# Kernel optimization log

Measured on AMD Instinct MI355X. Metric: run time of the kernel, lower is better.

Reference implementation:

```python
import jax, jax.numpy as jnp
import numpy as np

V, E, H, B, T1, T2 = 32000, 300, 300, 64, 48, 48


def _lstm_last(x, Wih, Whh, bih, bhh):
    # x: [T, B, in]; returns final hidden state h_T: [B, H] (PyTorch gate order i,f,g,o)
    h0 = jnp.zeros((x.shape[1], Whh.shape[1]), x.dtype)
    def step(carry, xt):
        h, c = carry
        g = xt @ Wih.T + h @ Whh.T + bih + bhh
        i, f, gc, o = jnp.split(g, 4, axis=-1)
        c = jax.nn.sigmoid(f) * c + jax.nn.sigmoid(i) * jnp.tanh(gc)
        h = jax.nn.sigmoid(o) * jnp.tanh(c)
        return (h, c), None
    (h, _), _ = jax.lax.scan(step, (h0, h0), x)
    return h


def _bilstm_last(x, pf, pr):
    hf = _lstm_last(x, *pf)
    hr = _lstm_last(x[::-1], *pr)
    # faithful quirk: original reverses projr[0] along dim 0 == BATCH dim
    return jnp.concatenate([hf, hr[::-1]], axis=1)  # [B, 2H]


def _forward(x1, x2, x1_mask, x2_mask,
             emb, eW, eU, ebi, ebh, rW, rU, rbi, rbh,
             dW, dU, dbi, dbh, sW, sU, sbi, sbh,
             f1w, f1b, f2w, f2b, fow, fob):
    emb1 = emb[x1]  # [T1,B,E]
    emb2 = emb[x2]
    # encoder outputs final hidden [B,2H], broadcast over time by mask multiply (faithful quirk)
    ctx1 = _bilstm_last(emb1, (eW, eU, ebi, ebh), (rW, rU, rbi, rbh))[None] * x1_mask[:, :, None]  # [T1,B,2H]
    ctx2 = _bilstm_last(emb2, (eW, eU, ebi, ebh), (rW, rU, rbi, rbh))[None] * x2_mask[:, :, None]  # [T2,B,2H]
    c1 = ctx1.transpose(1, 0, 2)  # [B,T1,2H]
    c2 = ctx2.transpose(1, 0, 2)  # [B,T2,2H]
    # scores[b,i,j] = max_d c1[b,i,d]*c2[b,j,d]  (vectorized form of the O(T1*T2) python loop)
    scores = jnp.max(c1[:, :, None, :] * c2[:, None, :, :], axis=-1)  # [B,T1,T2]
    m1 = x1_mask.T  # [B,T1]
    m2 = x2_mask.T  # [B,T2]
    # masked softmax over hypothesis axis (axis=2)
    ea = jnp.exp(scores - jnp.max(scores, axis=2, keepdims=True)) * m2[:, None, :]
    alpha = ea / jnp.sum(ea, axis=2, keepdims=True)  # [B,T1,T2]
    # faithful quirk: MAX (not sum) pooling of attention-weighted hypothesis
    a_tilde = jnp.max(alpha[:, :, :, None] * c2[:, None, :, :], axis=2)  # [B,T1,2H]
    # masked softmax over premise axis (axis=1)
    eb = jnp.exp(scores - jnp.max(scores, axis=1, keepdims=True)) * m1[:, :, None]
    beta = eb / jnp.sum(eb, axis=1, keepdims=True)  # [B,T1,T2]
    b_tilde = jnp.einsum('bij,bid->bjd', beta, c1)  # [B,T2,2H]
    ctx1_ = a_tilde.transpose(1, 0, 2)  # [T1,B,2H]
    ctx2_ = b_tilde.transpose(1, 0, 2)  # [T2,B,2H]
    inp1 = jnp.concatenate([ctx1, ctx1_, ctx1 * ctx1_, ctx1 - ctx1_], axis=2)  # [T1,B,8H]
    inp2 = jnp.concatenate([ctx2, ctx2_, ctx2 * ctx2_, ctx2 - ctx2_], axis=2)
    h1 = jax.nn.relu(inp1 @ f1w.T + f1b)
    h2 = jax.nn.relu(inp2 @ f1w.T + f1b)
    ctx3 = _bilstm_last(h1, (dW, dU, dbi, dbh), (sW, sU, sbi, sbh))  # [B,2H]
    ctx4 = _bilstm_last(h2, (dW, dU, dbi, dbh), (sW, sU, sbi, sbh))  # [B,2H]
    w3 = ctx3[None] * x1_mask[:, :, None]  # [T1,B,2H]
    w4 = ctx4[None] * x2_mask[:, :, None]  # [T2,B,2H]
    logit = jnp.concatenate([
        w3.sum(0) / x1_mask.sum(0)[:, None], w3.max(0),
        w4.sum(0) / x2_mask.sum(0)[:, None], w4.max(0)], axis=1)  # [B,8H]
    logit = jnp.tanh(logit @ f2w.T + f2b)
    return logit @ fow.T + fob  # [B,3]


def setup_inputs() -> dict:
    key = jax.random.key(0)
    ks = jax.random.split(key, 32)
    s = 0.05
    n = lambda k, shape: jax.random.normal(k, shape, jnp.float32) * s
    d = {
        'x1': jax.random.randint(ks[0], (T1, B), 0, V, dtype=jnp.int32),
        'x1_mask': jnp.ones((T1, B), jnp.float32),
        'x2': jax.random.randint(ks[1], (T2, B), 0, V, dtype=jnp.int32),
        'x2_mask': jnp.ones((T2, B), jnp.float32),
        'l': T1,
        'embed_table': n(ks[2], (V, E)),
        'enc_Wih': n(ks[3], (4 * H, E)), 'enc_Whh': n(ks[4], (4 * H, H)),
        'enc_bih': n(ks[5], (4 * H,)), 'enc_bhh': n(ks[6], (4 * H,)),
        'encr_Wih': n(ks[7], (4 * H, E)), 'encr_Whh': n(ks[8], (4 * H, H)),
        'encr_bih': n(ks[9], (4 * H,)), 'encr_bhh': n(ks[10], (4 * H,)),
        'dec_Wih': n(ks[11], (4 * H, H)), 'dec_Whh': n(ks[12], (4 * H, H)),
        'dec_bih': n(ks[13], (4 * H,)), 'dec_bhh': n(ks[14], (4 * H,)),
        'decr_Wih': n(ks[15], (4 * H, H)), 'decr_Whh': n(ks[16], (4 * H, H)),
        'decr_bih': n(ks[17], (4 * H,)), 'decr_bhh': n(ks[18], (4 * H,)),
        'fc1_w': n(ks[19], (H, 8 * H)), 'fc1_b': n(ks[20], (H,)),
        'fc2_w': n(ks[21], (H, 8 * H)), 'fc2_b': n(ks[22], (H,)),
        'fco_w': n(ks[23], (3, H)), 'fco_b': n(ks[24], (3,)),
    }
    return d


def reference(x1, x1_mask, x2, x2_mask, l, embed_table,
              enc_Wih, enc_Whh, enc_bih, enc_bhh,
              encr_Wih, encr_Whh, encr_bih, encr_bhh,
              dec_Wih, dec_Whh, dec_bih, dec_bhh,
              decr_Wih, decr_Whh, decr_bih, decr_bhh,
              fc1_w, fc1_b, fc2_w, fc2_b, fco_w, fco_b):
    del l  # unused in original forward
    return _forward(x1, x2, x1_mask, x2_mask, embed_table,
                    enc_Wih, enc_Whh, enc_bih, enc_bhh,
                    encr_Wih, encr_Whh, encr_bih, encr_bhh,
                    dec_Wih, dec_Whh, dec_bih, dec_bhh,
                    decr_Wih, decr_Whh, decr_bih, decr_bhh,
                    fc1_w, fc1_b, fc2_w, fc2_b, fco_w, fco_b)
```

## Files before the change

kernel.cpp:

```cpp
#include <hip/hip_runtime.h>
#include <math.h>

typedef unsigned short u16;
typedef unsigned int u32;
typedef unsigned long long u64;
typedef __attribute__((ext_vector_type(8))) __bf16 bf16x8;
typedef __attribute__((ext_vector_type(4))) float f32x4;
typedef __attribute__((ext_vector_type(4))) _Float16 f16x4;

#define MR   6144
#define KP1  320
#define NPG  1280
#define NG   1200
#define WSEG 409600
#define UPSEG 409600
#define GT_H 163840

#define OFF_ABF    0UL
#define OFF_WBF    3932160UL
#define OFF_WCF    10485760UL
#define OFF_BIAS   12645760UL
#define OFF_GF     12664960UL
#define OFF_GR     28393600UL
#define OFF_HB     44122240UL
#define OFF_ENC    44286080UL
#define OFF_VB     44593280UL
#define OFF_CO     45822080UL
#define OFF_ATT    46436480UL
#define OFF_PT     46473344UL
#define OFF_LG     47087744UL
#define OFF_UP     47164544UL

#define HX_BYTES   655360UL

__device__ __forceinline__ float fsig(float x) { return 1.0f / (1.0f + __expf(-x)); }
__device__ __forceinline__ float ftanh(float x) { return 1.0f - 2.0f / (__expf(2.0f * x) + 1.0f); }

__device__ __forceinline__ u16 f2bf(float x) {
    union { float f; u32 u; } v; v.f = x;
    u32 r = v.u + 0x7fffu + ((v.u >> 16) & 1u);
    return (u16)(r >> 16);
}
__device__ __forceinline__ float bf2f(u16 x) {
    union { u32 u; float f; } v; v.u = ((u32)x) << 16; return v.f;
}

__device__ __forceinline__ void gld_lds16(const u16* g, u16* l) {
    __builtin_amdgcn_global_load_lds(
        (const __attribute__((address_space(1))) unsigned int*)g,
        (__attribute__((address_space(3))) unsigned int*)l, 16, 0, 0);
}

#define PREP_B0 7680
#define PREP_B1 14080
#define PREP_B2 20480
#define PREP_B3 20499
#define PREP_B4 22609
__global__ __launch_bounds__(256) void prep_k(
    const int* __restrict__ x1, const int* __restrict__ x2, const float* __restrict__ emb,
    const float* __restrict__ w0, const float* __restrict__ w1,
    const float* __restrict__ w2, const float* __restrict__ w3,
    const float* __restrict__ u0, const float* __restrict__ u1,
    const float* __restrict__ u2, const float* __restrict__ u3,
    const float* __restrict__ b0i, const float* __restrict__ b0h,
    const float* __restrict__ b1i, const float* __restrict__ b1h,
    const float* __restrict__ b2i, const float* __restrict__ b2h,
    const float* __restrict__ b3i, const float* __restrict__ b3h,
    const float* __restrict__ f1w,
    u16* __restrict__ abf, u16* __restrict__ wbf, u16* __restrict__ up,
    float* __restrict__ bias, float* __restrict__ wc) {
    int bid = blockIdx.x;
    if (bid < PREP_B0) {
        int idx = bid * 256 + threadIdx.x;
        int r = idx / KP1, k = idx % KP1;
        float v = 0.0f;
        if (k < 300) {
            int t = r >> 7, bc = r & 127;
            int tok = (bc < 64) ? x1[t * 64 + bc] : x2[t * 64 + bc - 64];
            v = emb[tok * 300 + k];
        }
        abf[idx] = f2bf(v);
    } else if (bid < PREP_B1) {
        int idx = (bid - PREP_B0) * 256 + threadIdx.x;
        int s = idx / (NPG * KP1), rem = idx % (NPG * KP1);
        int r = rem / KP1, k = rem % KP1;
        const float* w = (s == 0) ? w0 : (s == 1) ? w1 : (s == 2) ? w2 : w3;
        float v = 0.0f;
        if (r < NG && k < 300) {
            int j = r >> 2, g = r & 3;
            v = w[(g * 300 + j) * 300 + k];
        }
        wbf[idx] = f2bf(v);
    } else if (bid < PREP_B2) {
        int idx = (bid - PREP_B1) * 256 + threadIdx.x;
        int seg = idx / UPSEG, pos = idx % UPSEG;
        int T = pos / 5120, kt = (pos / 512) % 10, l = (pos >> 3) & 63, e = pos & 7;
        int n = T * 16 + (l & 15);
        int k = kt * 32 + (l >> 4) * 8 + e;
        const float* us = (seg == 0) ? u0 : (seg == 1) ? u1 : (seg == 2) ? u2 : u3;
        float v = 0.0f;
        if (n < NG && k < 300) {
            int j = n >> 2, g = n & 3;
            v = us[(g * 300 + j) * 300 + k];
        }
        up[idx] = f2bf(v);
    } else if (bid < PREP_B3) {
        int idx = (bid - PREP_B2) * 256 + threadIdx.x;
        if (idx < 4 * NG) {
            int s = idx / NG, n = idx % NG;
            int j = n >> 2, g = n & 3;
            int src = g * 300 + j;
            const float* bi = (s == 0) ? b0i : (s == 1) ? b1i : (s == 2) ? b2i : b3i;
            const float* bh = (s == 0) ? b0h : (s == 1) ? b1h : (s == 2) ? b2h : b3h;
            bias[idx] = bi[src] + bh[src];
        }
    } else {
        int idx = (bid - PREP_B3) * 256 + threadIdx.x;
        if (idx < 300 * 1800) {
            int n = idx / 1800, k = idx % 1800;
            int nk = n * 2400 + k;
            float v;
            if (k < 600)       v = f1w[nk] + f1w[nk + 1800];
            else if (k < 1200) v = f1w[nk] - f1w[nk + 1200];
            else               v = f1w[nk];
            wc[idx] = v;
        }
    }
}

__global__ __launch_bounds__(256) void gemm_bt(const u16* __restrict__ A,
                                               const u16* __restrict__ Wb,
                                               const float* __restrict__ biasb,
                                               _Float16* __restrict__ G0,
                                               _Float16* __restrict__ G1) {
    __shared__ __align__(16) u16 smA[128 * 32];
    __shared__ __align__(16) u16 smB[128 * 32];
    int sidx = blockIdx.z;
    const u16* B = Wb + (size_t)sidx * WSEG;
    const float* bias = biasb + sidx * NG;
    _Float16* Gh = sidx ? G1 : G0;
    int m0 = blockIdx.x * 128, n0 = blockIdx.y * 128;
    int tid = threadIdx.x, ln = tid & 63;
    int wm = (tid >> 6) & 1, wn = tid >> 7;
    int lrow = ln & 15, lq = ln >> 4;
    f32x4 acc[4][4] = {};
    for (int k0 = 0; k0 < KP1; k0 += 32) {
#pragma unroll
        for (int p = 0; p < 2; p++) {
            int e = (p * 256 + tid) * 8;
            int r = e >> 5, kk = e & 31;
            gld_lds16(A + (size_t)(m0 + r) * KP1 + k0 + kk, smA + e);
            gld_lds16(B + (size_t)(n0 + r) * KP1 + k0 + kk, smB + e);
        }
        __syncthreads();
        bf16x8 av[4], bv[4];
#pragma unroll
        for (int i = 0; i < 4; i++) {
            av[i] = *(const bf16x8*)&smA[(wm * 64 + i * 16 + lrow) * 32 + lq * 8];
            bv[i] = *(const bf16x8*)&smB[(wn * 64 + i * 16 + lrow) * 32 + lq * 8];
        }
#pragma unroll
        for (int i = 0; i < 4; i++)
#pragma unroll
            for (int j = 0; j < 4; j++)
                acc[i][j] = __builtin_amdgcn_mfma_f32_16x16x32_bf16(av[i], bv[j], acc[i][j], 0, 0, 0);
        __syncthreads();
    }
    size_t tb = (size_t)blockIdx.x * GT_H + (size_t)blockIdx.y * 16384
              + (size_t)wm * 8192 + (size_t)wn * 2048 + (size_t)ln * 4;
#pragma unroll
    for (int i = 0; i < 4; i++)
#pragma unroll
        for (int j = 0; j < 4; j++) {
            int n = n0 + wn * 64 + j * 16 + lrow;
            f16x4 v;
            if (n < NG) {
                float bb = bias[n];
#pragma unroll
                for (int r = 0; r < 4; r++) v[r] = (_Float16)(acc[i][j][r] + bb);
            } else {
                v = (f16x4)0;
            }
            *(f16x4*)(Gh + tb + (size_t)(i >> 1) * 4096 + (size_t)(((i & 1) * 4 + j)) * 256) = v;
        }
}

__global__ __launch_bounds__(256, 1) void lstm_sync(const _Float16* __restrict__ Gf,
                                                    const _Float16* __restrict__ Gr,
                                                    const u16* __restrict__ Upf,
                                                    const u16* __restrict__ Upr,
                                                    u64* __restrict__ hx,
                                                    u16* __restrict__ hb) {
    int nt = blockIdx.x, dir = blockIdx.y, half = blockIdx.z;
    const _Float16* G = dir ? Gr : Gf;
    const u16* Up = dir ? Upr : Upf;

    int tid = threadIdx.x, ln = tid & 63, w = tid >> 6;
    int wm = w & 1, wn = w >> 1;
    int lrow = ln & 15, lq = ln >> 4;

    __shared__ __align__(16) u16 Ulds[80 * 512];
    __shared__ __align__(16) u32 Hst[64 * 160];
    __shared__ float P[64][132];

    for (int p = 0; p < 20; p++) {
        int e = (p * 256 + tid) * 8;
        gld_lds16(Up + (size_t)nt * 40960 + e, Ulds + e);
    }
    __syncthreads();

    u32* HOw = (u32*)hb;

    int jp = tid & 15, bg = tid >> 4;
    float c[4][2];
#pragma unroll
    for (int q = 0; q < 4; q++) { c[q][0] = 0.0f; c[q][1] = 0.0f; }

    const _Float16* Gs = G + (size_t)nt * 16384 + (size_t)half * 8192
                       + (size_t)wm * 4096 + (size_t)wn * 2048 + (size_t)ln * 4;
    f16x4 gpre[8];
    {
        int ttg = dir ? 47 : 0;
        const _Float16* Gt = Gs + (size_t)ttg * GT_H;
#pragma unroll
        for (int f = 0; f < 8; f++) gpre[f] = *(const f16x4*)(Gt + (size_t)f * 256);
    }

    for (int t = 0; t < 48; t++) {
        {
            const u64* slab = hx + ((size_t)(t & 1) * 2 + dir) * 20480 + (size_t)half * 10240;
            u32 want = (u32)t;
            u32 hv[40];
            for (;;) {
                bool ok = true;
#pragma unroll
                for (int q = 0; q < 40; q++) {
                    u64 x = __hip_atomic_load(slab + q * 256 + tid,
                                              __ATOMIC_RELAXED, __HIP_MEMORY_SCOPE_AGENT);
                    hv[q] = (u32)x;
                    ok &= ((u32)(x >> 32) == want);
                }
                if (ok) break;
                __builtin_amdgcn_s_sleep(1);
            }
#pragma unroll
            for (int q = 0; q < 40; q++) {
                int idx = q * 256 + tid;
                int row = idx / 160, cc = idx - row * 160;
                Hst[row * 160 + (cc ^ ((row & 7) << 2))] = hv[q];
            }
        }
        __syncthreads();

        f32x4 acc[2][4];
#pragma unroll
        for (int i = 0; i < 2; i++)
#pragma unroll
            for (int j = 0; j < 4; j++) {
                f32x4 a;
#pragma unroll
                for (int r = 0; r < 4; r++) a[r] = (float)gpre[i * 4 + j][r];
                acc[i][j] = a;
            }

#pragma unroll
        for (int kt = 0; kt < 10; kt++) {
            bf16x8 av[2], bv[4];
#pragma unroll
            for (int i = 0; i < 2; i++) {
                int row = wm * 32 + i * 16 + lrow;
                int cc = (kt * 16 + lq * 4) ^ ((row & 7) << 2);
                av[i] = *(const bf16x8*)&Hst[row * 160 + cc];
            }
#pragma unroll
            for (int j = 0; j < 4; j++)
                bv[j] = *(const bf16x8*)&Ulds[((size_t)(wn * 4 + j) * 10 + kt) * 512 + ln * 8];
#pragma unroll
            for (int i = 0; i < 2; i++)
#pragma unroll
                for (int j = 0; j < 4; j++)
                    acc[i][j] = __builtin_amdgcn_mfma_f32_16x16x32_bf16(av[i], bv[j], acc[i][j], 0, 0, 0);
        }

#pragma unroll
        for (int i = 0; i < 2; i++)
#pragma unroll
            for (int j = 0; j < 4; j++) {
                int col = wn * 64 + j * 16 + lrow;
#pragma unroll
                for (int r = 0; r < 4; r++)
                    P[wm * 32 + i * 16 + lq * 4 + r][col] = acc[i][j][r];
            }
        __syncthreads();

        if (t < 47) {
            int ttg = dir ? 46 - t : t + 1;
            const _Float16* Gt = Gs + (size_t)ttg * GT_H;
#pragma unroll
            for (int f = 0; f < 8; f++) gpre[f] = *(const f16x4*)(Gt + (size_t)f * 256);
        }

        {
            u64* hxo = hx + ((size_t)((t + 1) & 1) * 2 + dir) * 20480;
            u64 tagb = ((u64)(u32)(t + 1)) << 32;
#pragma unroll
            for (int q = 0; q < 4; q++) {
                int bc = bg * 4 + q;
                f32x4 g0 = *(const f32x4*)&P[bc][8 * jp];
                f32x4 g1 = *(const f32x4*)&P[bc][8 * jp + 4];
                float cn0 = fsig(g0[1]) * c[q][0] + fsig(g0[0]) * ftanh(g0[2]);
                float hn0 = fsig(g0[3]) * ftanh(cn0);
                float cn1 = fsig(g1[1]) * c[q][1] + fsig(g1[0]) * ftanh(g1[2]);
                float hn1 = fsig(g1[3]) * ftanh(cn1);
                c[q][0] = cn0; c[q][1] = cn1;
                u32 pk = (u32)f2bf(hn0) | ((u32)f2bf(hn1) << 16);
                int bcg = half * 64 + bc;
                size_t oi = (size_t)bcg * 160 + nt * 16 + jp;
                if (t < 47)
                    __hip_atomic_store(hxo + oi, (u64)pk | tagb,
                                       __ATOMIC_RELAXED, __HIP_MEMORY_SCOPE_AGENT);
                else
                    HOw[(size_t)dir * 20480 + oi] = pk;
            }
        }
    }
}

__global__ __launch_bounds__(256) void enc_k(const u16* __restrict__ hF,
                                             const u16* __restrict__ hR,
                                             float* __restrict__ enc) {
    int idx = blockIdx.x * 256 + threadIdx.x;
    if (idx >= 128 * 600) return;
    int bc = idx / 600, d = idx % 600;
    int seq = bc >> 6, b = bc & 63;
    enc[idx] = (d < 300) ? bf2f(hF[bc * KP1 + d])
                         : bf2f(hR[(seq * 64 + 63 - b) * KP1 + d - 300]);
}

__global__ __launch_bounds__(256) void vbuf_k(const float* __restrict__ enc,
                                              float* __restrict__ V) {
    int idx = blockIdx.x * 256 + threadIdx.x;
    if (idx >= 64 * 600) return;
    int b = idx / 600, d = idx % 600;
    float e1 = enc[b * 600 + d], e2 = enc[(64 + b) * 600 + d];
    float p = fmaxf(e2, 0.0f), nn = fminf(e2, 0.0f);
    V[0 * 38400 + idx] = e1;
    V[1 * 38400 + idx] = p;
    V[2 * 38400 + idx] = nn;
    V[3 * 38400 + idx] = e1 * p;
    V[4 * 38400 + idx] = e1 * nn;
    V[5 * 38400 + idx] = e2;
    V[6 * 38400 + idx] = e1;
    V[7 * 38400 + idx] = e1 * e2;
}

__global__ __launch_bounds__(256) void attn_lite(const float* __restrict__ enc,
                                                 const float* __restrict__ x1m,
                                                 const float* __restrict__ x2m,
                                                 float* __restrict__ AMX,
                                                 float* __restrict__ AMN,
                                                 float* __restrict__ SS) {
    int b = blockIdx.x, tid = threadIdx.x;
    __shared__ float sc[48][49];
    __shared__ float rmx[4], rmn[4];
    __shared__ float MxMn[2];
    float mx = -3.4e38f, mn = 3.4e38f;
    for (int d = tid; d < 600; d += 256) {
        float p = enc[b * 600 + d] * enc[(64 + b) * 600 + d];
        mx = fmaxf(mx, p); mn = fminf(mn, p);
    }
    for (int off = 32; off; off >>= 1) {
        mx = fmaxf(mx, __shfl_down(mx, off));
        mn = fminf(mn, __shfl_down(mn, off));
    }
    if ((tid & 63) == 0) { rmx[tid >> 6] = mx; rmn[tid >> 6] = mn; }
    __syncthreads();
    if (tid == 0) {
        MxMn[0] = fmaxf(fmaxf(rmx[0], rmx[1]), fmaxf(rmx[2], rmx[3]));
        MxMn[1] = fminf(fminf(rmn[0], rmn[1]), fminf(rmn[2], rmn[3]));
    }
    __syncthreads();
    float Mx = MxMn[0], Mn = MxMn[1];
    for (int idx = tid; idx < 2304; idx += 256) {
        int i = idx / 48, j = idx % 48;
        float q = x1m[i * 64 + b] * x2m[j * 64 + b];
        sc[i][j] = (q > 0.0f) ? q * Mx : ((q < 0.0f) ? q * Mn : 0.0f);
    }
    __syncthreads();
    if (tid < 48) {
        int i = tid;
        float m = -3.4e38f;
        for (int j = 0; j < 48; j++) m = fmaxf(m, sc[i][j]);
        float sum = 0.0f;
        for (int j = 0; j < 48; j++) sum += expf(sc[i][j] - m) * x2m[j * 64 + b];
        float wmax = -3.4e38f, wmin = 3.4e38f;
        for (int j = 0; j < 48; j++) {
            float w = expf(sc[i][j] - m) * x2m[j * 64 + b] * x2m[j * 64 + b];
            wmax = fmaxf(wmax, w); wmin = fminf(wmin, w);
        }
        AMX[i * 64 + b] = wmax / sum;
        AMN[i * 64 + b] = wmin / sum;
    } else if (tid >= 64 && tid < 112) {
        int j = tid - 64;
        float m = -3.4e38f;
        for (int i = 0; i < 48; i++) m = fmaxf(m, sc[i][j]);
        float sum = 0.0f, sm = 0.0f;
        for (int i = 0; i < 48; i++) {
            float e = expf(sc[i][j] - m) * x1m[i * 64 + b];
            sum += e; sm += e * x1m[i * 64 + b];
        }
        SS[j * 64 + b] = sm / sum;
    }
}

__global__ __launch_bounds__(256) void coeff_gemm(const float* __restrict__ V,
                                                  const float* __restrict__ Wc,
                                                  float* __restrict__ CO) {
    __shared__ float As[16][64];
    __shared__ float Ws[16][64];
    int s = blockIdx.y;
    const int offs[8] = {0, 600, 600, 1200, 1200, 0, 600, 1200};
    int koff = offs[s];
    const float* A = V + (size_t)s * 38400;
    float* C = CO + (size_t)s * 19200;
    int n0 = blockIdx.x * 64;
    int tid = threadIdx.x;
    int lrow = tid >> 2;
    int lk4 = (tid & 3) << 2;
    int tm = (tid & 15) << 2;
    int tn = (tid >> 4) << 2;
    int nW = n0 + lrow;
    float acc[4][4] = {};
    for (int k0 = 0; k0 < 600; k0 += 16) {
        __syncthreads();
#pragma unroll
        for (int q = 0; q < 4; q++) {
            int k = k0 + lk4 + q;
            As[lk4 + q][lrow] = (k < 600) ? A[lrow * 600 + k] : 0.0f;
            Ws[lk4 + q][lrow] = (k < 600 && nW < 300) ? Wc[(size_t)nW * 1800 + koff + k] : 0.0f;
        }
        __syncthreads();
#pragma unroll
        for (int kk = 0; kk < 16; kk++) {
            float a0 = As[kk][tm], a1 = As[kk][tm + 1], a2 = As[kk][tm + 2], a3 = As[kk][tm + 3];
            float w0 = Ws[kk][tn], w1 = Ws[kk][tn + 1], w2 = Ws[kk][tn + 2], w3 = Ws[kk][tn + 3];
            acc[0][0] += a0 * w0; acc[0][1] += a0 * w1; acc[0][2] += a0 * w2; acc[0][3] += a0 * w3;
            acc[1][0] += a1 * w0; acc[1][1] += a1 * w1; acc[1][2] += a1 * w2; acc[1][3] += a1 * w3;
            acc[2][0] += a2 * w0; acc[2][1] += a2 * w1; acc[2][2] += a2 * w2; acc[2][3] += a2 * w3;
            acc[3][0] += a3 * w0; acc[3][1] += a3 * w1; acc[3][2] += a3 * w2; acc[3][3] += a3 * w3;
        }
    }
#pragma unroll
    for (int ii = 0; ii < 4; ii++) {
        int m = tm + ii;
#pragma unroll
        for (int jn = 0; jn < 4; jn++) {
            int n = n0 + tn + jn;
            if (n < 300) C[m * 300 + n] = acc[ii][jn];
        }
    }
}

__global__ __launch_bounds__(320) void combine_k(const float* __restrict__ CO,
                                                 const float* __restrict__ f1b,
                                                 const float* __restrict__ x1m,
                                                 const float* __restrict__ x2m,
                                                 const float* __restrict__ AMX,
                                                 const float* __restrict__ AMN,
                                                 const float* __restrict__ SS,
                                                 u16* __restrict__ OUT) {
    int r = blockIdx.x;
    int t = r >> 7, bc = r & 127;
    int seq = bc >> 6, b = bc & 63;
    int n = threadIdx.x;
    if (n >= 300) return;
    int bn = b * 300 + n;
    float pre;
    if (seq == 0) {
        float m1 = x1m[t * 64 + b], am = AMX[t * 64 + b], an = AMN[t * 64 + b];
        pre = m1 * CO[bn] + am * CO[19200 + bn] + an * CO[2 * 19200 + bn]
            + m1 * am * CO[3 * 19200 + bn] + m1 * an * CO[4 * 19200 + bn] + f1b[n];
    } else {
        float m2 = x2m[t * 64 + b], sv = SS[t * 64 + b];
        pre = m2 * CO[5 * 19200 + bn] + sv * CO[6 * 19200 + bn]
            + m2 * sv * CO[7 * 19200 + bn] + f1b[n];
    }
    OUT[(size_t)r * KP1 + n] = f2bf(fmaxf(pre, 0.0f));
}

__global__ __launch_bounds__(256) void pool_k(const float* __restrict__ dctx,
                                              const float* __restrict__ x1m,
                                              const float* __restrict__ x2m,
                                              float* __restrict__ pooledT) {
    int idx = blockIdx.x * 256 + threadIdx.x;
    if (idx >= 64 * 2400) return;
    int b = idx / 2400, col = idx % 2400;
    int sec = col / 600, d = col % 600;
    const float* msk = (sec < 2) ? x1m : x2m;
    float v = dctx[((sec < 2 ? 0 : 64) + b) * 600 + d];
    float out;
    if ((sec & 1) == 0) {
        float s = 0, sm = 0;
        for (int t = 0; t < 48; t++) { float mv = msk[t * 64 + b]; s += v * mv; sm += mv; }
        out = s / sm;
    } else {
        float m = -3.4e38f;
        for (int t = 0; t < 48; t++) m = fmaxf(m, v * msk[t * 64 + b]);
        out = m;
    }
    pooledT[col * 64 + b] = out;
}

__global__ __launch_bounds__(256) void fc2_k2(const float* __restrict__ pooledT,
                                              const float* __restrict__ f2w,
                                              const float* __restrict__ f2b,
                                              float* __restrict__ logit) {
    __shared__ float wl[2400];
    __shared__ float red[256];
    int n = blockIdx.x;
    for (int i = threadIdx.x; i < 2400; i += 256) wl[i] = f2w[n * 2400 + i];
    __syncthreads();
    int b = threadIdx.x & 63, kc = threadIdx.x >> 6;
    float acc = 0.0f;
    int k0 = kc * 600;
    for (int kk = 0; kk < 600; kk++) acc += pooledT[(k0 + kk) * 64 + b] * wl[k0 + kk];
    red[threadIdx.x] = acc;
    __syncthreads();
    if (threadIdx.x < 64) {
        float s = red[b] + red[64 + b] + red[128 + b] + red[192 + b];
        logit[b * 300 + n] = tanhf(s + f2b[n]);
    }
}

__global__ __launch_bounds__(64) void out_k2(const float* __restrict__ logit,
                                             const float* __restrict__ fow,
                                             const float* __restrict__ fob,
                                             float* __restrict__ out) {
    int b = blockIdx.x, tid = threadIdx.x;
    float p0 = 0, p1 = 0, p2 = 0;
    for (int k = tid; k < 300; k += 64) {
        float l = logit[b * 300 + k];
        p0 += l * fow[k]; p1 += l * fow[300 + k]; p2 += l * fow[600 + k];
    }
    for (int off = 32; off; off >>= 1) {
        p0 += __shfl_down(p0, off);
        p1 += __shfl_down(p1, off);
        p2 += __shfl_down(p2, off);
    }
    if (tid == 0) {
        out[b * 3 + 0] = p0 + fob[0];
        out[b * 3 + 1] = p1 + fob[1];
        out[b * 3 + 2] = p2 + fob[2];
    }
}

extern "C" void kernel_launch(void* const* d_in, const int* in_sizes, int n_in,
                              void* d_out, int out_size, void* d_ws, size_t ws_size,
                              hipStream_t stream) {
    (void)in_sizes; (void)n_in; (void)out_size; (void)ws_size;
    const int*   x1  = (const int*)d_in[0];
    const float* x1m = (const float*)d_in[1];
    const int*   x2  = (const int*)d_in[2];
    const float* x2m = (const float*)d_in[3];
    const float* emb = (const float*)d_in[5];
    const float* eW  = (const float*)d_in[6];
    const float* eU  = (const float*)d_in[7];
    const float* ebi = (const float*)d_in[8];
    const float* ebh = (const float*)d_in[9];
    const float* rW  = (const float*)d_in[10];
    const float* rU  = (const float*)d_in[11];
    const float* rbi = (const float*)d_in[12];
    const float* rbh = (const float*)d_in[13];
    const float* dW  = (const float*)d_in[14];
    const float* dU  = (const float*)d_in[15];
    const float* dbi = (const float*)d_in[16];
    const float* dbh = (const float*)d_in[17];
    const float* sW  = (const float*)d_in[18];
    const float* sU  = (const float*)d_in[19];
    const float* sbi = (const float*)d_in[20];
    const float* sbh = (const float*)d_in[21];
    const float* f1w = (const float*)d_in[22];
    const float* f1b = (const float*)d_in[23];
    const float* f2w = (const float*)d_in[24];
    const float* f2b = (const float*)d_in[25];
    const float* fow = (const float*)d_in[26];
    const float* fob = (const float*)d_in[27];

    char* wsb = (char*)d_ws;
    u16*       ABF  = (u16*)(wsb + OFF_ABF);
    u16*       WBF  = (u16*)(wsb + OFF_WBF);
    float*     WCF  = (float*)(wsb + OFF_WCF);
    float*     BIAS = (float*)(wsb + OFF_BIAS);
    _Float16*  GFh  = (_Float16*)(wsb + OFF_GF);
    _Float16*  GRh  = (_Float16*)(wsb + OFF_GR);
    u16*       HB   = (u16*)(wsb + OFF_HB);
    float*     ENC  = (float*)(wsb + OFF_ENC);
    float*     VB   = (float*)(wsb + OFF_VB);
    float*     CO   = (float*)(wsb + OFF_CO);
    float*     AMX  = (float*)(wsb + OFF_ATT);
    float*     AMN  = AMX + 3072;
    float*     SS   = AMX + 6144;
    float*     PT   = (float*)(wsb + OFF_PT);
    float*     LG   = (float*)(wsb + OFF_LG);
    u16*       UP   = (u16*)(wsb + OFF_UP);
    u64*       HX64 = (u64*)(wsb + OFF_ABF);

    u16* HF0 = HB;
    u16* HR0 = HB + 40960;

    prep_k<<<dim3(PREP_B4), 256, 0, stream>>>(
        x1, x2, emb, eW, rW, dW, sW, eU, rU, dU, sU,
        ebi, ebh, rbi, rbh, dbi, dbh, sbi, sbh, f1w,
        ABF, WBF, UP, BIAS, WCF);

    gemm_bt<<<dim3(48, 10, 2), 256, 0, stream>>>(ABF, WBF, BIAS, GFh, GRh);
    hipMemsetAsync(wsb + OFF_ABF, 0, HX_BYTES, stream);
    lstm_sync<<<dim3(10, 2, 2), 256, 0, stream>>>(GFh, GRh, UP, UP + UPSEG, HX64, HB);

    enc_k<<<dim3((128 * 600 + 255) / 256), 256, 0, stream>>>(HF0, HR0, ENC);
    vbuf_k<<<dim3((64 * 600 + 255) / 256), 256, 0, stream>>>(ENC, VB);
    attn_lite<<<dim3(64), 256, 0, stream>>>(ENC, x1m, x2m, AMX, AMN, SS);
    coeff_gemm<<<dim3(5, 8), 256, 0, stream>>>(VB, WCF, CO);
    combine_k<<<dim3(6144), 320, 0, stream>>>(CO, f1b, x1m, x2m, AMX, AMN, SS, ABF);

    gemm_bt<<<dim3(48, 10, 2), 256, 0, stream>>>(ABF, WBF + 2 * WSEG, BIAS + 2 * NG, GFh, GRh);
    hipMemsetAsync(wsb + OFF_ABF, 0, HX_BYTES, stream);
    lstm_sync<<<dim3(10, 2, 2), 256, 0, stream>>>(GFh, GRh, UP + 2 * UPSEG, UP + 3 * UPSEG, HX64, HB);

    enc_k<<<dim3((128 * 600 + 255) / 256), 256, 0, stream>>>(HF0, HR0, ENC);
    pool_k<<<dim3((64 * 2400 + 255) / 256), 256, 0, stream>>>(ENC, x1m, x2m, PT);
    fc2_k2<<<dim3(300), 256, 0, stream>>>(PT, f2w, f2b, LG);
    out_k2<<<dim3(64), 64, 0, stream>>>(LG, fow, fob, (float*)d_out);
}
```

Before: 856.6 us.

## Fuse encoder gather into consumers and pre-poll subset of hidden-state tags

Removes the two enc_k launches and the fp32 ENC buffer by having vbuf_k, attn_lite and pool_k read the bf16 final hidden states directly through an inline gather helper. This cuts two small kernel launches and a round trip through global memory. The LSTM step also first spins on a small subset of the tagged hidden-state slab before loading all 40 entries, so fewer wide atomic loads are repeated while waiting. Consumers now redo the index and bf16 conversion arithmetic themselves.

```diff
diff --git a/kernel.cpp b/kernel.cpp
--- a/kernel.cpp
+++ b/kernel.cpp
@@ -23,7 +23,6 @@
 #define OFF_GF     12664960UL
 #define OFF_GR     28393600UL
 #define OFF_HB     44122240UL
-#define OFF_ENC    44286080UL
 #define OFF_VB     44593280UL
 #define OFF_CO     45822080UL
 #define OFF_ATT    46436480UL
@@ -43,6 +42,11 @@
 }
 __device__ __forceinline__ float bf2f(u16 x) {
     union { u32 u; float f; } v; v.u = ((u32)x) << 16; return v.f;
+}
+
+__device__ __forceinline__ float encread(const u16* hF, const u16* hR, int bc, int d) {
+    return (d < 300) ? bf2f(hF[bc * KP1 + d])
+                     : bf2f(hR[((bc >> 6) * 64 + 63 - (bc & 63)) * KP1 + d - 300]);
 }
 
 __device__ __forceinline__ void gld_lds16(const u16* g, u16* l) {
@@ -230,6 +234,17 @@
         {
             const u64* slab = hx + ((size_t)(t & 1) * 2 + dir) * 20480 + (size_t)half * 10240;
             u32 want = (u32)t;
+            for (;;) {
+                bool pok = true;
+#pragma unroll
+                for (int q = 0; q < 5; q++) {
+                    u64 x = __hip_atomic_load(slab + q * 256 + tid,
+                                              __ATOMIC_RELAXED, __HIP_MEMORY_SCOPE_AGENT);
+                    pok &= ((u32)(x >> 32) == want);
+                }
+                if (pok) break;
+                __builtin_amdgcn_s_sleep(1);
+            }
             u32 hv[40];
             for (;;) {
                 bool ok = true;
@@ -326,23 +341,13 @@
     }
 }
 
-__global__ __launch_bounds__(256) void enc_k(const u16* __restrict__ hF,
-                                             const u16* __restrict__ hR,
-                                             float* __restrict__ enc) {
-    int idx = blockIdx.x * 256 + threadIdx.x;
-    if (idx >= 128 * 600) return;
-    int bc = idx / 600, d = idx % 600;
-    int seq = bc >> 6, b = bc & 63;
-    enc[idx] = (d < 300) ? bf2f(hF[bc * KP1 + d])
-                         : bf2f(hR[(seq * 64 + 63 - b) * KP1 + d - 300]);
-}
-
-__global__ __launch_bounds__(256) void vbuf_k(const float* __restrict__ enc,
+__global__ __launch_bounds__(256) void vbuf_k(const u16* __restrict__ hF,
+                                              const u16* __restrict__ hR,
                                               float* __restrict__ V) {
     int idx = blockIdx.x * 256 + threadIdx.x;
     if (idx >= 64 * 600) return;
     int b = idx / 600, d = idx % 600;
-    float e1 = enc[b * 600 + d], e2 = enc[(64 + b) * 600 + d];
+    float e1 = encread(hF, hR, b, d), e2 = encread(hF, hR, 64 + b, d);
     float p = fmaxf(e2, 0.0f), nn = fminf(e2, 0.0f);
     V[0 * 38400 + idx] = e1;
     V[1 * 38400 + idx] = p;
@@ -354,7 +359,8 @@
     V[7 * 38400 + idx] = e1 * e2;
 }
 
-__global__ __launch_bounds__(256) void attn_lite(const float* __restrict__ enc,
+__global__ __launch_bounds__(256) void attn_lite(const u16* __restrict__ hF,
+                                                 const u16* __restrict__ hR,
                                                  const float* __restrict__ x1m,
                                                  const float* __restrict__ x2m,
                                                  float* __restrict__ AMX,
@@ -366,7 +372,7 @@
     __shared__ float MxMn[2];
     float mx = -3.4e38f, mn = 3.4e38f;
     for (int d = tid; d < 600; d += 256) {
-        float p = enc[b * 600 + d] * enc[(64 + b) * 600 + d];
+        float p = encread(hF, hR, b, d) * encread(hF, hR, 64 + b, d);
         mx = fmaxf(mx, p); mn = fminf(mn, p);
     }
     for (int off = 32; off; off >>= 1) {
@@ -488,7 +494,8 @@
     OUT[(size_t)r * KP1 + n] = f2bf(fmaxf(pre, 0.0f));
 }
 
-__global__ __launch_bounds__(256) void pool_k(const float* __restrict__ dctx,
+__global__ __launch_bounds__(256) void pool_k(const u16* __restrict__ hF,
+                                              const u16* __restrict__ hR,
                                               const float* __restrict__ x1m,
                                               const float* __restrict__ x2m,
                                               float* __restrict__ pooledT) {
@@ -497,7 +504,7 @@
     int b = idx / 2400, col = idx % 2400;
     int sec = col / 600, d = col % 600;
     const float* msk = (sec < 2) ? x1m : x2m;
-    float v = dctx[((sec < 2 ? 0 : 64) + b) * 600 + d];
+    float v = encread(hF, hR, (sec < 2 ? 0 : 64) + b, d);
     float out;
     if ((sec & 1) == 0) {
         float s = 0, sm = 0;
@@ -594,7 +601,6 @@
     _Float16*  GFh  = (_Float16*)(wsb + OFF_GF);
     _Float16*  GRh  = (_Float16*)(wsb + OFF_GR);
     u16*       HB   = (u16*)(wsb + OFF_HB);
-    float*     ENC  = (float*)(wsb + OFF_ENC);
     float*     VB   = (float*)(wsb + OFF_VB);
     float*     CO   = (float*)(wsb + OFF_CO);
     float*     AMX  = (float*)(wsb + OFF_ATT);
@@ -617,9 +623,8 @@
     hipMemsetAsync(wsb + OFF_ABF, 0, HX_BYTES, stream);
     lstm_sync<<<dim3(10, 2, 2), 256, 0, stream>>>(GFh, GRh, UP, UP + UPSEG, HX64, HB);
 
-    enc_k<<<dim3((128 * 600 + 255) / 256), 256, 0, stream>>>(HF0, HR0, ENC);
-    vbuf_k<<<dim3((64 * 600 + 255) / 256), 256, 0, stream>>>(ENC, VB);
-    attn_lite<<<dim3(64), 256, 0, stream>>>(ENC, x1m, x2m, AMX, AMN, SS);
+    vbuf_k<<<dim3((64 * 600 + 255) / 256), 256, 0, stream>>>(HF0, HR0, VB);
+    attn_lite<<<dim3(64), 256, 0, stream>>>(HF0, HR0, x1m, x2m, AMX, AMN, SS);
     coeff_gemm<<<dim3(5, 8), 256, 0, stream>>>(VB, WCF, CO);
     combine_k<<<dim3(6144), 320, 0, stream>>>(CO, f1b, x1m, x2m, AMX, AMN, SS, ABF);
 
@@ -627,8 +632,7 @@
     hipMemsetAsync(wsb + OFF_ABF, 0, HX_BYTES, stream);
     lstm_sync<<<dim3(10, 2, 2), 256, 0, stream>>>(GFh, GRh, UP + 2 * UPSEG, UP + 3 * UPSEG, HX64, HB);
 
-    enc_k<<<dim3((128 * 600 + 255) / 256), 256, 0, stream>>>(HF0, HR0, ENC);
-    pool_k<<<dim3((64 * 2400 + 255) / 256), 256, 0, stream>>>(ENC, x1m, x2m, PT);
+    pool_k<<<dim3((64 * 2400 + 255) / 256), 256, 0, stream>>>(HF0, HR0, x1m, x2m, PT);
     fc2_k2<<<dim3(300), 256, 0, stream>>>(PT, f2w, f2b, LG);
     out_k2<<<dim3(64), 64, 0, stream>>>(LG, fow, fob, (float*)d_out);
 }
```

New measurement: 860.5 us. Within noise of the previous version (+0.5%).
